# Optimization experiments

Hardware: AMD Instinct MI355X
Metric: run time of the kernel (lower is better)

The kernel has to match this reference:

```python
import jax, jax.numpy as jnp
import numpy as np


def setup_inputs() -> dict:
    key = jax.random.key(0)
    k1, k2 = jax.random.split(key)
    B, S, E, V = 8, 512, 512, 50000
    batch = jax.random.normal(k1, (B, S, E), dtype=jnp.float32)
    emb = jax.random.normal(k2, (V, E), dtype=jnp.float32)
    return {"batch": batch, "emb": emb}


def reference(batch, emb):
    # __init__ with distance != 'L2': embedding table is L2-normalized once.
    emb_n = emb / jnp.linalg.norm(emb, axis=1, keepdims=True)  # [V, E]
    # forward: normalize batch along last (emb) dim.
    b = batch / jnp.linalg.norm(batch, axis=2, keepdims=True)  # [B, S, E]
    B, S, E = b.shape
    # cosine_distance: flatten tokens, GEMM against table, 1 - sim, argmin over V.
    mult = b.reshape(-1, E) @ emb_n.T            # [B*S, V]
    cosine_dist = 1.0 - mult
    nearest = jnp.argmin(cosine_dist, axis=1)    # [B*S]
    return nearest.reshape(B, S)
```

## Files before the change

kernel.cpp:

```cpp
#include <hip/hip_runtime.h>
#include <stdint.h>

typedef _Float16 f16;
typedef _Float16 f16x4 __attribute__((ext_vector_type(4)));
typedef _Float16 f16x8 __attribute__((ext_vector_type(8)));
typedef float    f32x4 __attribute__((ext_vector_type(4)));

__device__ __forceinline__ void llds16(const void* g, void* l) {
    __builtin_amdgcn_global_load_lds(
        (const __attribute__((address_space(1))) void*)g,
        (__attribute__((address_space(3))) void*)l, 16, 0, 0);
}

__device__ __forceinline__ unsigned long long pack_key(float s, int j) {
    unsigned u = __float_as_uint(s);
    u = (u & 0x80000000u) ? ~u : (u | 0x80000000u);
    return ((unsigned long long)u << 32) | (unsigned)(~(unsigned)j);
}

__global__ void convert_emb_kernel(const float* __restrict__ emb,
                                   f16* __restrict__ bh,
                                   float* __restrict__ rinv, int V, int E) {
    int row  = blockIdx.x * (blockDim.x >> 6) + (threadIdx.x >> 6);
    int lane = threadIdx.x & 63;
    if (row >= V) return;
    const float4* p = (const float4*)(emb + (size_t)row * E);
    int n4 = E >> 2;
    float ss = 0.f;
    for (int i = lane; i < n4; i += 64) {
        float4 v = p[i];
        ss = fmaf(v.x, v.x, ss); ss = fmaf(v.y, v.y, ss);
        ss = fmaf(v.z, v.z, ss); ss = fmaf(v.w, v.w, ss);
    }
    #pragma unroll
    for (int o = 32; o > 0; o >>= 1) ss += __shfl_down(ss, o, 64);
    if (lane == 0) rinv[row] = 1.0f / sqrtf(ss);

    for (int i = lane; i < n4; i += 64) {
        float4 v = p[i];
        f16x4 h;
        h.x = (f16)v.x; h.y = (f16)v.y; h.z = (f16)v.z; h.w = (f16)v.w;
        *(f16x4*)&bh[(size_t)row * E + i * 4] = h;
    }
}

__global__ void convert_batch_kernel(const float* __restrict__ batch,
                                     f16* __restrict__ ah, int M, int E) {
    int row  = blockIdx.x * (blockDim.x >> 6) + (threadIdx.x >> 6);
    int lane = threadIdx.x & 63;
    if (row >= M) return;
    const float4* p = (const float4*)(batch + (size_t)row * E);
    int n4 = E >> 2;
    for (int i = lane; i < n4; i += 64) {
        float4 v = p[i];
        f16x4 h;
        h.x = (f16)v.x; h.y = (f16)v.y; h.z = (f16)v.z; h.w = (f16)v.w;
        *(f16x4*)&ah[(size_t)row * E + i * 4] = h;
    }
}

__global__ void init_bmax_kernel(unsigned* __restrict__ bmax, int n) {
    int i = blockIdx.x * blockDim.x + threadIdx.x;
    for (; i < n; i += gridDim.x * blockDim.x) bmax[i] = 0u;
}

#define BM 256
#define BN 128
#define BKH 64

__global__ __launch_bounds__(512, 4) void nn_hh_kernel(
    const f16* __restrict__ Ah, const f16* __restrict__ Bh,
    const float* __restrict__ rinvP, unsigned* __restrict__ bmax,
    int M, int V, int E, int NG)
{
    __shared__ f16 sA[BM * BKH];
    __shared__ f16 sB[BN * BKH];

    const int tid  = threadIdx.x;
    const int lane = tid & 63;
    const int w    = tid >> 6;
    const int wr   = w >> 1;
    const int wc   = w & 1;
    const int fr   = lane & 15;
    const int kg   = lane >> 4;

    const int row0 = blockIdx.x * BM;
    const int col0 = blockIdx.y * BN;

    const int srow  = lane >> 3;
    const int sslot = lane & 7;
    const int xslot = sslot ^ srow;
    int aoff[4], ldofA[4];
    #pragma unroll
    for (int it = 0; it < 4; ++it) {
        int rl = w * 32 + it * 8 + srow;
        aoff[it]  = (row0 + rl) * E + xslot * 8;
        ldofA[it] = (w * 32 + it * 8) * BKH;
    }
    int boff[2], ldofB[2];
    #pragma unroll
    for (int it = 0; it < 2; ++it) {
        int rl = w * 16 + it * 8 + srow;
        int bj = col0 + rl; if (bj > V - 1) bj = V - 1;
        boff[it]  = bj * E + xslot * 8;
        ldofB[it] = (w * 16 + it * 8) * BKH;
    }

    f32x4 acc[4][4];
    #pragma unroll
    for (int m = 0; m < 4; ++m)
        #pragma unroll
        for (int n = 0; n < 4; ++n) acc[m][n] = (f32x4){0.f, 0.f, 0.f, 0.f};

    const int steps = E / BKH;
    for (int ks = 0; ks < steps; ++ks) {
        const int kadv = ks * BKH;
        #pragma unroll
        for (int it = 0; it < 4; ++it)
            llds16(Ah + aoff[it] + kadv, sA + ldofA[it]);
        #pragma unroll
        for (int it = 0; it < 2; ++it)
            llds16(Bh + boff[it] + kadv, sB + ldofB[it]);
        __syncthreads();

        #pragma unroll
        for (int ksub = 0; ksub < 2; ++ksub) {
            f16x8 ah[4], bh[4];
            #pragma unroll
            for (int m = 0; m < 4; ++m) {
                int row = wr * 64 + m * 16 + fr;
                int off = row * BKH + (((ksub * 4 + kg) ^ (fr & 7)) << 3);
                ah[m] = *(const f16x8*)&sA[off];
            }
            #pragma unroll
            for (int n = 0; n < 4; ++n) {
                int col = wc * 64 + n * 16 + fr;
                int off = col * BKH + (((ksub * 4 + kg) ^ (fr & 7)) << 3);
                bh[n] = *(const f16x8*)&sB[off];
            }
            #pragma unroll
            for (int m = 0; m < 4; ++m)
                #pragma unroll
                for (int n = 0; n < 4; ++n)
                    acc[m][n] = __builtin_amdgcn_mfma_f32_16x16x32_f16(
                        ah[m], bh[n], acc[m][n], 0, 0, 0);
        }
        __syncthreads();
    }

    const int colb = col0 + wc * 64;
    const int g    = colb >> 6;
    float ri[4];
    #pragma unroll
    for (int n = 0; n < 4; ++n) {
        int j = colb + n * 16 + fr;
        ri[n] = (j < V) ? rinvP[j] : 0.f;
    }
    #pragma unroll
    for (int m = 0; m < 4; ++m) {
        #pragma unroll
        for (int r = 0; r < 4; ++r) {
            float best = -3.4e38f;
            #pragma unroll
            for (int n = 0; n < 4; ++n) {
                int j = colb + n * 16 + fr;
                float sc = (j < V) ? acc[m][n][r] * ri[n] : -3.4e38f;
                best = fmaxf(best, sc);
            }
            #pragma unroll
            for (int o = 8; o > 0; o >>= 1)
                best = fmaxf(best, __shfl_xor(best, o, 64));
            if (fr == 0) {
                int row = row0 + wr * 64 + m * 16 + kg * 4 + r;
                unsigned u = __float_as_uint(best);
                u = (u & 0x80000000u) ? ~u : (u | 0x80000000u);
                atomicMax(&bmax[(size_t)row * NG + g], u);
            }
        }
    }
}

#define TAU 0.008f
#define NGMAX 800

__global__ __launch_bounds__(256) void refine_kernel(
    const float* __restrict__ batch, const float* __restrict__ emb,
    const float* __restrict__ rinvP, const unsigned* __restrict__ bmax,
    int* __restrict__ out, int V, int E, int NG)
{
    const int r   = blockIdx.x;
    const int tid = threadIdx.x;
    __shared__ float arow[512];
    __shared__ float gv[NGMAX];
    __shared__ float part[4][64];
    __shared__ int   lst[NGMAX];
    __shared__ int   cnt;
    __shared__ float wmax[4];

    for (int i = tid; i < E; i += 256) arow[i] = batch[(size_t)r * E + i];
    if (tid == 0) cnt = 0;

    float lm = -3.4e38f;
    for (int g = tid; g < NG; g += 256) {
        unsigned u = bmax[(size_t)r * NG + g];
        unsigned v = (u & 0x80000000u) ? (u & 0x7FFFFFFFu) : ~u;
        float f = __uint_as_float(v);
        gv[g] = f;
        lm = fmaxf(lm, f);
    }
    #pragma unroll
    for (int o = 32; o > 0; o >>= 1) lm = fmaxf(lm, __shfl_xor(lm, o, 64));
    if ((tid & 63) == 0) wmax[tid >> 6] = lm;
    __syncthreads();
    const float m1 = fmaxf(fmaxf(wmax[0], wmax[1]), fmaxf(wmax[2], wmax[3]));
    const float thresh = m1 - TAU;

    for (int g = tid; g < NG; g += 256)
        if (gv[g] >= thresh) { int i = atomicAdd(&cnt, 1); lst[i] = g; }
    __syncthreads();
    const int n = cnt;

    const int colL = tid & 63;
    const int kq   = tid >> 6;
    unsigned long long best = 0ULL;
    for (int li = 0; li < n; ++li) {
        const int j = lst[li] * 64 + colL;
        float p = 0.f;
        if (j < V) {
            const float4* bp = (const float4*)(emb + (size_t)j * E + kq * 128);
            const float4* ap = (const float4*)(&arow[kq * 128]);
            #pragma unroll 8
            for (int i = 0; i < 32; ++i) {
                float4 b = bp[i], a = ap[i];
                p = fmaf(a.x, b.x, p); p = fmaf(a.y, b.y, p);
                p = fmaf(a.z, b.z, p); p = fmaf(a.w, b.w, p);
            }
        }
        part[kq][colL] = p;
        __syncthreads();
        if (kq == 0 && j < V) {
            float dot = (part[0][colL] + part[1][colL]) +
                        (part[2][colL] + part[3][colL]);
            unsigned long long key = pack_key(dot * rinvP[j], j);
            if (key > best) best = key;
        }
        __syncthreads();
    }

    if (tid < 64) {
        #pragma unroll
        for (int o = 32; o > 0; o >>= 1) {
            unsigned long long other = __shfl_xor(best, o, 64);
            if (other > best) best = other;
        }
        if (tid == 0) out[r] = (int)(~(unsigned)(best & 0xFFFFFFFFULL));
    }
}

__global__ void init_keys_kernel(unsigned long long* __restrict__ keys, int M) {
    int i = blockIdx.x * blockDim.x + threadIdx.x;
    if (i < M) keys[i] = 0ULL;
}

__global__ void extract_kernel(const unsigned long long* __restrict__ keys,
                               int* __restrict__ out, int M) {
    int i = blockIdx.x * blockDim.x + threadIdx.x;
    if (i < M) out[i] = (int)(~(unsigned)(keys[i] & 0xFFFFFFFFULL));
}

__global__ void inv_norms_kernel(const float* __restrict__ emb,
                                 float* __restrict__ r, int V, int E) {
    int row  = blockIdx.x * (blockDim.x >> 6) + (threadIdx.x >> 6);
    int lane = threadIdx.x & 63;
    if (row >= V) return;
    const float4* p = reinterpret_cast<const float4*>(emb + (size_t)row * E);
    float ss = 0.f;
    int n4 = E >> 2;
    for (int i = lane; i < n4; i += 64) {
        float4 v = p[i];
        ss = fmaf(v.x, v.x, ss); ss = fmaf(v.y, v.y, ss);
        ss = fmaf(v.z, v.z, ss); ss = fmaf(v.w, v.w, ss);
    }
    #pragma unroll
    for (int o = 32; o > 0; o >>= 1) ss += __shfl_down(ss, o, 64);
    if (lane == 0) r[row] = 1.0f / sqrtf(ss);
}

#define FBM 128
#define FBN 128
#define FBK 32
#define LDSPAD 4

__global__ __launch_bounds__(256) void nn_gemm_argmax(
    const float* __restrict__ batch, const float* __restrict__ emb,
    const float* __restrict__ rinv, unsigned long long* __restrict__ keys,
    int M, int V, int E)
{
    __shared__ float As[FBK][FBM + LDSPAD];
    __shared__ float Bs[FBK][FBN + LDSPAD];
    const int tid = threadIdx.x;
    const int tx  = tid & 15;
    const int ty  = tid >> 4;
    const int row0 = blockIdx.y * FBM;
    const int col0 = blockIdx.x * FBN;
    float acc[8][8];
    #pragma unroll
    for (int i = 0; i < 8; ++i)
        #pragma unroll
        for (int j = 0; j < 8; ++j) acc[i][j] = 0.f;
    const int steps = E / FBK;
    for (int ks = 0; ks < steps; ++ks) {
        const int k0 = ks * FBK;
        #pragma unroll
        for (int it = 0; it < 4; ++it) {
            int idx = it * 256 + tid;
            int rr = idx >> 3, cc = idx & 7;
            float4 v = *reinterpret_cast<const float4*>(
                &batch[(size_t)(row0 + rr) * E + k0 + cc * 4]);
            As[cc*4+0][rr] = v.x; As[cc*4+1][rr] = v.y;
            As[cc*4+2][rr] = v.z; As[cc*4+3][rr] = v.w;
        }
        #pragma unroll
        for (int it = 0; it < 4; ++it) {
            int idx = it * 256 + tid;
            int rr = idx >> 3, cc = idx & 7;
            int j = col0 + rr;
            float4 v = make_float4(0.f,0.f,0.f,0.f);
            if (j < V)
                v = *reinterpret_cast<const float4*>(&emb[(size_t)j * E + k0 + cc * 4]);
            Bs[cc*4+0][rr] = v.x; Bs[cc*4+1][rr] = v.y;
            Bs[cc*4+2][rr] = v.z; Bs[cc*4+3][rr] = v.w;
        }
        __syncthreads();
        #pragma unroll
        for (int k = 0; k < FBK; ++k) {
            float4 a0 = *reinterpret_cast<const float4*>(&As[k][ty*8]);
            float4 a1 = *reinterpret_cast<const float4*>(&As[k][ty*8+4]);
            float4 b0 = *reinterpret_cast<const float4*>(&Bs[k][tx*8]);
            float4 b1 = *reinterpret_cast<const float4*>(&Bs[k][tx*8+4]);
            float a[8] = {a0.x,a0.y,a0.z,a0.w,a1.x,a1.y,a1.z,a1.w};
            float b[8] = {b0.x,b0.y,b0.z,b0.w,b1.x,b1.y,b1.z,b1.w};
            #pragma unroll
            for (int i = 0; i < 8; ++i)
                #pragma unroll
                for (int jj = 0; jj < 8; ++jj)
                    acc[i][jj] = fmaf(a[i], b[jj], acc[i][jj]);
        }
        __syncthreads();
    }
    #pragma unroll
    for (int i = 0; i < 8; ++i) {
        const int q = row0 + ty * 8 + i;
        unsigned long long best = 0ULL;
        #pragma unroll
        for (int jj = 0; jj < 8; ++jj) {
            int j = col0 + tx * 8 + jj;
            if (j < V) {
                unsigned long long key = pack_key(acc[i][jj] * rinv[j], j);
                if (key > best) best = key;
            }
        }
        #pragma unroll
        for (int o = 8; o > 0; o >>= 1) {
            unsigned long long other = __shfl_xor(best, o, 64);
            if (other > best) best = other;
        }
        if (tx == 0 && best != 0ULL) atomicMax(&keys[q], best);
    }
}

extern "C" void kernel_launch(void* const* d_in, const int* in_sizes, int n_in,
                              void* d_out, int out_size, void* d_ws, size_t ws_size,
                              hipStream_t stream) {
    const float* batch = (const float*)d_in[0];
    const float* emb   = (const float*)d_in[1];
    int* out = (int*)d_out;

    const int M = out_size;
    const int E = in_sizes[0] / M;
    const int V = in_sizes[1] / E;
    const int NG = (V + 63) / 64;

    auto al256 = [](size_t x) { return (x + 255) & ~(size_t)255; };
    size_t o_rinv = 0;
    size_t o_keys = al256(o_rinv + (size_t)V * 4);
    size_t o_bmax = al256(o_keys + (size_t)M * 8);
    size_t o_Ah   = al256(o_bmax + (size_t)M * NG * 4);
    size_t o_Bh   = al256(o_Ah  + (size_t)M * E * 2);
    size_t need   = al256(o_Bh  + (size_t)V * E * 2);

    float* rinv = (float*)((char*)d_ws + o_rinv);
    unsigned long long* keys = (unsigned long long*)((char*)d_ws + o_keys);
    unsigned* bmax = (unsigned*)((char*)d_ws + o_bmax);

    if (ws_size >= need && E == 512 && (M % BM) == 0 && NG <= NGMAX) {
        f16* Ah = (f16*)((char*)d_ws + o_Ah);
        f16* Bh = (f16*)((char*)d_ws + o_Bh);

        convert_emb_kernel<<<(V + 3) / 4, 256, 0, stream>>>(emb, Bh, rinv, V, E);
        convert_batch_kernel<<<(M + 3) / 4, 256, 0, stream>>>(batch, Ah, M, E);
        init_bmax_kernel<<<2048, 256, 0, stream>>>(bmax, M * NG);

        dim3 grid(M / BM, (V + BN - 1) / BN);
        nn_hh_kernel<<<grid, 512, 0, stream>>>(Ah, Bh, rinv, bmax, M, V, E, NG);

        refine_kernel<<<M, 256, 0, stream>>>(batch, emb, rinv, bmax, out, V, E, NG);
    } else {
        inv_norms_kernel<<<(V + 3) / 4, 256, 0, stream>>>(emb, rinv, V, E);
        init_keys_kernel<<<(M + 255) / 256, 256, 0, stream>>>(keys, M);
        dim3 grid((V + FBN - 1) / FBN, M / FBM);
        nn_gemm_argmax<<<grid, 256, 0, stream>>>(batch, emb, rinv, keys, M, V, E);
        extract_kernel<<<(M + 255) / 256, 256, 0, stream>>>(keys, out, M);
    }
}
```

Before: 388.6 us.

## Double-buffer LDS tiles with halved K step and MFMA priority boost

Shrinks the K tile from 64 to 32 and double-buffers the A/B shared-memory tiles, so global-to-LDS loads for the next step are issued while MFMAs run on the current one. The per-step barrier count drops from two to one, and the swizzle pattern is rebuilt for the 4-slot row. s_setprio is raised around the MFMA block. The cost is twice as many K iterations, each with less work. There is also a possible race: the async global_load_lds into the alternate buffer is not explicitly waited on before the barrier.

```diff
diff --git a/kernel.cpp b/kernel.cpp
--- a/kernel.cpp
+++ b/kernel.cpp
@@ -66,15 +66,15 @@
 
 #define BM 256
 #define BN 128
-#define BKH 64
+#define BKH 32
 
 __global__ __launch_bounds__(512, 4) void nn_hh_kernel(
     const f16* __restrict__ Ah, const f16* __restrict__ Bh,
     const float* __restrict__ rinvP, unsigned* __restrict__ bmax,
     int M, int V, int E, int NG)
 {
-    __shared__ f16 sA[BM * BKH];
-    __shared__ f16 sB[BN * BKH];
+    __shared__ f16 sA[2][BM * BKH];
+    __shared__ f16 sB[2][BN * BKH];
 
     const int tid  = threadIdx.x;
     const int lane = tid & 63;
@@ -87,23 +87,22 @@
     const int row0 = blockIdx.x * BM;
     const int col0 = blockIdx.y * BN;
 
-    const int srow  = lane >> 3;
-    const int sslot = lane & 7;
-    const int xslot = sslot ^ srow;
-    int aoff[4], ldofA[4];
-    #pragma unroll
-    for (int it = 0; it < 4; ++it) {
-        int rl = w * 32 + it * 8 + srow;
-        aoff[it]  = (row0 + rl) * E + xslot * 8;
-        ldofA[it] = (w * 32 + it * 8) * BKH;
-    }
-    int boff[2], ldofB[2];
+    const int r4   = lane >> 2;
+    const int sl   = lane & 3;
+    const int xsl  = sl ^ ((r4 >> 1) & 3);
+    int aoff[2], ldofA[2];
     #pragma unroll
     for (int it = 0; it < 2; ++it) {
-        int rl = w * 16 + it * 8 + srow;
+        int rl = w * 32 + it * 16 + r4;
+        aoff[it]  = (row0 + rl) * E + xsl * 8;
+        ldofA[it] = (w * 32 + it * 16) * BKH;
+    }
+    int boff, ldofB;
+    {
+        int rl = w * 16 + r4;
         int bj = col0 + rl; if (bj > V - 1) bj = V - 1;
-        boff[it]  = bj * E + xslot * 8;
-        ldofB[it] = (w * 16 + it * 8) * BKH;
+        boff  = bj * E + xsl * 8;
+        ldofB = (w * 16) * BKH;
     }
 
     f32x4 acc[4][4];
@@ -113,39 +112,46 @@
         for (int n = 0; n < 4; ++n) acc[m][n] = (f32x4){0.f, 0.f, 0.f, 0.f};
 
     const int steps = E / BKH;
+    const int rslot = kg ^ ((fr >> 1) & 3);
+
+    llds16(Ah + aoff[0], &sA[0][ldofA[0]]);
+    llds16(Ah + aoff[1], &sA[0][ldofA[1]]);
+    llds16(Bh + boff,    &sB[0][ldofB]);
+    __syncthreads();
+
+    int cur = 0;
+    #pragma unroll 1
     for (int ks = 0; ks < steps; ++ks) {
-        const int kadv = ks * BKH;
-        #pragma unroll
-        for (int it = 0; it < 4; ++it)
-            llds16(Ah + aoff[it] + kadv, sA + ldofA[it]);
-        #pragma unroll
-        for (int it = 0; it < 2; ++it)
-            llds16(Bh + boff[it] + kadv, sB + ldofB[it]);
+        if (ks + 1 < steps) {
+            const int kadv = (ks + 1) * BKH;
+            llds16(Ah + aoff[0] + kadv, &sA[cur ^ 1][ldofA[0]]);
+            llds16(Ah + aoff[1] + kadv, &sA[cur ^ 1][ldofA[1]]);
+            llds16(Bh + boff    + kadv, &sB[cur ^ 1][ldofB]);
+        }
+
+        f16x8 ah[4], bh[4];
+        #pragma unroll
+        for (int m = 0; m < 4; ++m) {
+            int row = wr * 64 + m * 16 + fr;
+            ah[m] = *(const f16x8*)&sA[cur][row * BKH + rslot * 8];
+        }
+        #pragma unroll
+        for (int n = 0; n < 4; ++n) {
+            int col = wc * 64 + n * 16 + fr;
+            bh[n] = *(const f16x8*)&sB[cur][col * BKH + rslot * 8];
+        }
+
+        __builtin_amdgcn_s_setprio(1);
+        #pragma unroll
+        for (int m = 0; m < 4; ++m)
+            #pragma unroll
+            for (int n = 0; n < 4; ++n)
+                acc[m][n] = __builtin_amdgcn_mfma_f32_16x16x32_f16(
+                    ah[m], bh[n], acc[m][n], 0, 0, 0);
+        __builtin_amdgcn_s_setprio(0);
+
         __syncthreads();
-
-        #pragma unroll
-        for (int ksub = 0; ksub < 2; ++ksub) {
-            f16x8 ah[4], bh[4];
-            #pragma unroll
-            for (int m = 0; m < 4; ++m) {
-                int row = wr * 64 + m * 16 + fr;
-                int off = row * BKH + (((ksub * 4 + kg) ^ (fr & 7)) << 3);
-                ah[m] = *(const f16x8*)&sA[off];
-            }
-            #pragma unroll
-            for (int n = 0; n < 4; ++n) {
-                int col = wc * 64 + n * 16 + fr;
-                int off = col * BKH + (((ksub * 4 + kg) ^ (fr & 7)) << 3);
-                bh[n] = *(const f16x8*)&sB[off];
-            }
-            #pragma unroll
-            for (int m = 0; m < 4; ++m)
-                #pragma unroll
-                for (int n = 0; n < 4; ++n)
-                    acc[m][n] = __builtin_amdgcn_mfma_f32_16x16x32_f16(
-                        ah[m], bh[n], acc[m][n], 0, 0, 0);
-        }
-        __syncthreads();
+        cur ^= 1;
     }
 
     const int colb = col0 + wc * 64;
```

New measurement: 416.4 us. 7.2% more time.
